# Performance work log

Measured on AMD Instinct MI355X. Metric: run time of the kernel, lower is better.

Reference implementation:

```python
import jax, jax.numpy as jnp
import numpy as np

NUM_BINS = 32
NUM_HEADS = 4
CHANNELS = 128
HEAD_DIM = CHANNELS // NUM_HEADS
SCALE = HEAD_DIM ** -0.5
BN_EPS = 1e-5


def setup_inputs() -> dict:
    key = jax.random.key(0)
    ks = jax.random.split(key, 8)
    B = 8192
    x = jax.random.normal(ks[0], (B, CHANNELS, NUM_BINS), dtype=jnp.float32)
    qkv_w = jax.random.normal(ks[1], (3 * CHANNELS, CHANNELS), dtype=jnp.float32) * (1.0 / np.sqrt(CHANNELS))
    qkv_b = jax.random.normal(ks[2], (3 * CHANNELS,), dtype=jnp.float32) * 0.01
    out_w = jax.random.normal(ks[3], (CHANNELS, CHANNELS), dtype=jnp.float32) * (1.0 / np.sqrt(CHANNELS))
    out_b = jax.random.normal(ks[4], (CHANNELS,), dtype=jnp.float32) * 0.01
    rel_pos_emb = jax.random.normal(ks[5], (2 * NUM_BINS - 1, NUM_HEADS), dtype=jnp.float32) * 0.02
    gamma = jnp.ones((CHANNELS,), dtype=jnp.float32)
    beta = jnp.zeros((CHANNELS,), dtype=jnp.float32)
    return {"x": x, "qkv_w": qkv_w, "qkv_b": qkv_b, "out_w": out_w,
            "out_b": out_b, "rel_pos_emb": rel_pos_emb, "gamma": gamma, "beta": beta}


def _rel_pos_bias(rel_pos_emb, n):
    # pos_idx[i,j] = (j - i) + num_bins - 1, clamped
    pos = jnp.arange(n)
    idx = jnp.clip(pos[None, :] - pos[:, None] + NUM_BINS - 1, 0, 2 * NUM_BINS - 2)
    bias = rel_pos_emb[idx]            # [n, n, H]
    return jnp.transpose(bias, (2, 0, 1))  # [H, n, n]


def reference(x, qkv_w, qkv_b, out_w, out_b, rel_pos_emb, gamma, beta):
    B, C, N = x.shape
    residual = x
    # 1x1 conv == per-position matmul over channels
    qkv = jnp.einsum('oc,bcn->bon', qkv_w, x) + qkv_b[None, :, None]  # [B, 3C, N]
    q, k, v = jnp.split(qkv, 3, axis=1)
    def heads(t):  # [B, C, N] -> [B, H, N, D]
        return jnp.transpose(t.reshape(B, NUM_HEADS, HEAD_DIM, N), (0, 1, 3, 2))
    q, k, v = heads(q), heads(k), heads(v)
    attn = jnp.einsum('bhnd,bhmd->bhnm', q, k) * SCALE
    attn = attn + _rel_pos_bias(rel_pos_emb, N)[None]  # [B, H, N, N]
    attn = jax.nn.softmax(attn, axis=-1)
    out = jnp.einsum('bhnm,bhmd->bhnd', attn, v)       # [B, H, N, D]
    out = jnp.transpose(out, (0, 1, 3, 2)).reshape(B, C, N)
    out = jnp.einsum('oc,bcn->bon', out_w, out) + out_b[None, :, None]
    out = out + residual
    # BatchNorm1d (training-mode batch stats, biased variance), per-channel over (B, N)
    mean = jnp.mean(out, axis=(0, 2), keepdims=True)
    var = jnp.mean((out - mean) ** 2, axis=(0, 2), keepdims=True)
    out = (out - mean) / jnp.sqrt(var + BN_EPS)
    out = out * gamma[None, :, None] + beta[None, :, None]
    return out
```

## Files before the change

### kernel.cpp

```cpp
#include <hip/hip_runtime.h>
#include <hip/hip_bf16.h>

typedef unsigned short u16;
typedef __bf16 bf16x8 __attribute__((ext_vector_type(8)));
typedef float f32x4 __attribute__((ext_vector_type(4)));

#define CH 128
#define NB 32
#define SCALE_F 0.17677669529663687f

__device__ __forceinline__ u16 f2b(float f) {
  union { float f; unsigned u; } v; v.f = f;
  unsigned r = v.u + 0x7fffu + ((v.u >> 16) & 1u);
  return (u16)(r >> 16);
}

__global__ void prep_kernel(const float* __restrict__ qw, const float* __restrict__ ow,
                            u16* __restrict__ wq, u16* __restrict__ wo,
                            float* __restrict__ stats) {
  int t = blockIdx.x * 256 + threadIdx.x;
  if (t < 49152) wq[t] = f2b(qw[t]);
  if (t < 16384) wo[t] = f2b(ow[t]);
  if (t < 8192)  stats[t] = 0.0f;
}

__global__ __launch_bounds__(256, 4) void attn_kernel(
    const float* __restrict__ x, const u16* __restrict__ wq,
    const float* __restrict__ qkv_b, const u16* __restrict__ wo,
    const float* __restrict__ out_b, const float* __restrict__ rel,
    float* __restrict__ out, float* __restrict__ stats) {

  __shared__ __attribute__((aligned(16))) u16 sQKt[32 * 256];
  __shared__ __attribute__((aligned(16))) u16 sVn[4][32 * 40];
  __shared__ __attribute__((aligned(16))) u16 sPO[4][32 * 40];

  const int tid = threadIdx.x;
  const int w = tid >> 6, lane = tid & 63;
  const int g = lane >> 4, l15 = lane & 15;
  const int b = blockIdx.x, h = w;
  const float* xb = x + (size_t)b * (CH * NB);
  const f32x4 zf = {0.f, 0.f, 0.f, 0.f};

  const float relv = rel[(lane < 63 ? lane : 62) * 4 + h];

  f32x4 acc[6][2];
  #pragma unroll
  for (int tt = 0; tt < 6; ++tt)
    #pragma unroll
    for (int ct = 0; ct < 2; ++ct) acc[tt][ct] = zf;

  #pragma unroll
  for (int kk = 0; kk < 4; ++kk) {
    bf16x8 bfr[2];
    #pragma unroll
    for (int ct = 0; ct < 2; ++ct) {
      float xv[8];
      #pragma unroll
      for (int j = 0; j < 8; ++j)
        xv[j] = xb[(kk * 32 + 8 * g + j) * NB + 16 * ct + l15];
      union { bf16x8 v; unsigned u[4]; } uu;
      #pragma unroll
      for (int m = 0; m < 4; ++m)
        uu.u[m] = (unsigned)f2b(xv[2 * m]) | ((unsigned)f2b(xv[2 * m + 1]) << 16);
      bfr[ct] = uu.v;
    }
    #pragma unroll
    for (int tt = 0; tt < 6; ++tt) {
      const int part = tt >> 1, td = tt & 1;
      const int row = part * 128 + h * 32 + 16 * td + l15;
      bf16x8 afr = *(const bf16x8*)&wq[row * 128 + kk * 32 + 8 * g];
      acc[tt][0] = __builtin_amdgcn_mfma_f32_16x16x32_bf16(afr, bfr[0], acc[tt][0], 0, 0, 0);
      acc[tt][1] = __builtin_amdgcn_mfma_f32_16x16x32_bf16(afr, bfr[1], acc[tt][1], 0, 0, 0);
    }
  }

  #pragma unroll
  for (int tt = 0; tt < 6; ++tt) {
    const int part = tt >> 1, td = tt & 1;
    #pragma unroll
    for (int r = 0; r < 4; ++r) {
      const int d = 16 * td + 4 * g + r;
      const int orow = part * 128 + h * 32 + d;
      const float bias = qkv_b[orow];
      #pragma unroll
      for (int ct = 0; ct < 2; ++ct) {
        const int n = 16 * ct + l15;
        const u16 hv = f2b(acc[tt][ct][r] + bias);
        if (part < 2) sQKt[(n * 256 + orow) ^ ((n & 7) << 3)] = hv;
        else          sVn[w][d * 40 + n] = hv;
      }
    }
  }

  bf16x8 qf[2], kf[2];
  #pragma unroll
  for (int t2 = 0; t2 < 2; ++t2) {
    const int n = 16 * t2 + l15;
    qf[t2] = *(const bf16x8*)&sQKt[(n * 256 + h * 32 + 8 * g) ^ ((n & 7) << 3)];
    kf[t2] = *(const bf16x8*)&sQKt[(n * 256 + 128 + h * 32 + 8 * g) ^ ((n & 7) << 3)];
  }
  f32x4 sacc[2][2];
  #pragma unroll
  for (int tn = 0; tn < 2; ++tn)
    #pragma unroll
    for (int tm = 0; tm < 2; ++tm)
      sacc[tn][tm] = __builtin_amdgcn_mfma_f32_16x16x32_bf16(qf[tn], kf[tm], zf, 0, 0, 0);

  u16* sPw = sPO[w];
  #pragma unroll
  for (int tn = 0; tn < 2; ++tn) {
    #pragma unroll
    for (int r = 0; r < 4; ++r) {
      const int n = 16 * tn + 4 * g + r;
      float v0 = sacc[tn][0][r] * SCALE_F + __shfl(relv, l15 - n + 31);
      float v1 = sacc[tn][1][r] * SCALE_F + __shfl(relv, 16 + l15 - n + 31);
      float mx = fmaxf(v0, v1);
      #pragma unroll
      for (int msk = 1; msk < 16; msk <<= 1) mx = fmaxf(mx, __shfl_xor(mx, msk));
      float e0 = __expf(v0 - mx), e1 = __expf(v1 - mx);
      float sm = e0 + e1;
      #pragma unroll
      for (int msk = 1; msk < 16; msk <<= 1) sm += __shfl_xor(sm, msk);
      const float ri = 1.0f / sm;
      sPw[n * 40 + l15]      = f2b(e0 * ri);
      sPw[n * 40 + 16 + l15] = f2b(e1 * ri);
    }
  }

  bf16x8 pf[2], vf[2];
  #pragma unroll
  for (int t2 = 0; t2 < 2; ++t2) {
    pf[t2] = *(const bf16x8*)&sPw[(16 * t2 + l15) * 40 + 8 * g];
    vf[t2] = *(const bf16x8*)&sVn[w][(16 * t2 + l15) * 40 + 8 * g];
  }
  f32x4 oacc[2][2];
  #pragma unroll
  for (int tn = 0; tn < 2; ++tn)
    #pragma unroll
    for (int td = 0; td < 2; ++td)
      oacc[tn][td] = __builtin_amdgcn_mfma_f32_16x16x32_bf16(pf[tn], vf[td], zf, 0, 0, 0);

  __syncthreads();

  u16* sO = &sPO[0][0];
  #pragma unroll
  for (int tn = 0; tn < 2; ++tn)
    #pragma unroll
    for (int td = 0; td < 2; ++td)
      #pragma unroll
      for (int r = 0; r < 4; ++r) {
        const int n = 16 * tn + 4 * g + r;
        const int c = h * 32 + 16 * td + l15;
        sO[(n * 128 + c) ^ ((n & 7) << 3)] = f2b(oacc[tn][td][r]);
      }

  __syncthreads();

  f32x4 pacc[2][2];
  #pragma unroll
  for (int mi = 0; mi < 2; ++mi)
    #pragma unroll
    for (int ct = 0; ct < 2; ++ct) pacc[mi][ct] = zf;

  #pragma unroll
  for (int kk = 0; kk < 4; ++kk) {
    bf16x8 bfr[2];
    #pragma unroll
    for (int ct = 0; ct < 2; ++ct) {
      const int n = 16 * ct + l15;
      bfr[ct] = *(const bf16x8*)&sO[(n * 128 + kk * 32 + 8 * g) ^ ((n & 7) << 3)];
    }
    #pragma unroll
    for (int mi = 0; mi < 2; ++mi) {
      const int row = 32 * w + 16 * mi + l15;
      bf16x8 afr = *(const bf16x8*)&wo[row * 128 + kk * 32 + 8 * g];
      pacc[mi][0] = __builtin_amdgcn_mfma_f32_16x16x32_bf16(afr, bfr[0], pacc[mi][0], 0, 0, 0);
      pacc[mi][1] = __builtin_amdgcn_mfma_f32_16x16x32_bf16(afr, bfr[1], pacc[mi][1], 0, 0, 0);
    }
  }

  float* ob = out + (size_t)b * (CH * NB);
  #pragma unroll
  for (int mi = 0; mi < 2; ++mi) {
    #pragma unroll
    for (int r = 0; r < 4; ++r) {
      const int o = 32 * w + 16 * mi + 4 * g + r;
      const float bias = out_b[o];
      float ssum = 0.f, ssq = 0.f;
      #pragma unroll
      for (int ct = 0; ct < 2; ++ct) {
        const int n = 16 * ct + l15;
        const float val = pacc[mi][ct][r] + bias + xb[o * NB + n];
        ob[o * NB + n] = val;
        ssum += val; ssq += val * val;
      }
      #pragma unroll
      for (int msk = 1; msk < 16; msk <<= 1) {
        ssum += __shfl_xor(ssum, msk);
        ssq  += __shfl_xor(ssq, msk);
      }
      if (l15 == 0) {
        atomicAdd(&stats[(b & 31) * 128 + o], ssum);
        atomicAdd(&stats[4096 + (b & 31) * 128 + o], ssq);
      }
    }
  }
}

__global__ void bnstats_kernel(const float* __restrict__ stats,
                               const float* __restrict__ gamma,
                               const float* __restrict__ beta,
                               float* __restrict__ sc, float* __restrict__ sh,
                               float invM) {
  int c = threadIdx.x;
  if (c >= 128) return;
  float s = 0.f, q = 0.f;
  #pragma unroll 8
  for (int i = 0; i < 32; ++i) {
    s += stats[i * 128 + c];
    q += stats[4096 + i * 128 + c];
  }
  float mean = s * invM;
  float var  = q * invM - mean * mean;
  float rstd = rsqrtf(var + 1e-5f);
  float a = gamma[c] * rstd;
  sc[c] = a;
  sh[c] = beta[c] - mean * a;
}

__global__ __launch_bounds__(256) void bnapply_kernel(float* __restrict__ out,
                                                      const float* __restrict__ sc,
                                                      const float* __restrict__ sh,
                                                      int n4total) {
  int i = blockIdx.x * 256 + threadIdx.x;
  int stride = gridDim.x * 256;
  for (; i < n4total; i += stride) {
    int c = (i >> 3) & 127;
    float a = sc[c], d = sh[c];
    float4 v = ((float4*)out)[i];
    v.x = v.x * a + d;
    v.y = v.y * a + d;
    v.z = v.z * a + d;
    v.w = v.w * a + d;
    ((float4*)out)[i] = v;
  }
}

extern "C" void kernel_launch(void* const* d_in, const int* in_sizes, int n_in,
                              void* d_out, int out_size, void* d_ws, size_t ws_size,
                              hipStream_t stream) {
  const float* x     = (const float*)d_in[0];
  const float* qkv_w = (const float*)d_in[1];
  const float* qkv_b = (const float*)d_in[2];
  const float* out_w = (const float*)d_in[3];
  const float* out_b = (const float*)d_in[4];
  const float* rel   = (const float*)d_in[5];
  const float* gamma = (const float*)d_in[6];
  const float* beta  = (const float*)d_in[7];
  float* out = (float*)d_out;

  const int B = in_sizes[0] / (CH * NB);

  u16* wq = (u16*)d_ws;
  u16* wo = wq + 49152;
  float* stats = (float*)(wo + 16384);
  float* sc = stats + 8192;
  float* sh = sc + 128;

  prep_kernel<<<192, 256, 0, stream>>>(qkv_w, out_w, wq, wo, stats);
  attn_kernel<<<B, 256, 0, stream>>>(x, wq, qkv_b, wo, out_b, rel, out, stats);
  bnstats_kernel<<<1, 128, 0, stream>>>(stats, gamma, beta, sc, sh, 1.0f / (float)(B * NB));
  bnapply_kernel<<<2048, 256, 0, stream>>>(out, sc, sh, out_size / 4);
}
```

Before: 430.0 us.

## Store pre-BN output as bf16 scratch, shrink LDS, transpose scores, raise occupancy

```diff
diff --git a/kernel.cpp b/kernel.cpp
--- a/kernel.cpp
+++ b/kernel.cpp
@@ -2,6 +2,7 @@
 #include <hip/hip_bf16.h>
 
 typedef unsigned short u16;
+typedef unsigned int u32;
 typedef __bf16 bf16x8 __attribute__((ext_vector_type(8)));
 typedef float f32x4 __attribute__((ext_vector_type(4)));
 
@@ -9,10 +10,12 @@
 #define NB 32
 #define SCALE_F 0.17677669529663687f
 
-__device__ __forceinline__ u16 f2b(float f) {
-  union { float f; unsigned u; } v; v.f = f;
-  unsigned r = v.u + 0x7fffu + ((v.u >> 16) & 1u);
-  return (u16)(r >> 16);
+__device__ __forceinline__ u16 b2u(__bf16 h) {
+  union { __bf16 h; u16 u; } v; v.h = h; return v.u;
+}
+__device__ __forceinline__ u16 f2b(float f) { return b2u((__bf16)f); }
+__device__ __forceinline__ u32 pk2(float lo, float hi) {
+  union { __bf16 h[2]; u32 w; } v; v.h[0] = (__bf16)lo; v.h[1] = (__bf16)hi; return v.w;
 }
 
 __global__ void prep_kernel(const float* __restrict__ qw, const float* __restrict__ ow,
@@ -24,15 +27,14 @@
   if (t < 8192)  stats[t] = 0.0f;
 }
 
-__global__ __launch_bounds__(256, 4) void attn_kernel(
+__global__ __launch_bounds__(256, 6) void attn_kernel(
     const float* __restrict__ x, const u16* __restrict__ wq,
     const float* __restrict__ qkv_b, const u16* __restrict__ wo,
     const float* __restrict__ out_b, const float* __restrict__ rel,
-    float* __restrict__ out, float* __restrict__ stats) {
-
-  __shared__ __attribute__((aligned(16))) u16 sQKt[32 * 256];
-  __shared__ __attribute__((aligned(16))) u16 sVn[4][32 * 40];
-  __shared__ __attribute__((aligned(16))) u16 sPO[4][32 * 40];
+    float* __restrict__ out, float* __restrict__ stats,
+    u16* __restrict__ preb) {
+
+  __shared__ __attribute__((aligned(16))) u16 pool[13312];
 
   const int tid = threadIdx.x;
   const int w = tid >> 6, lane = tid & 63;
@@ -41,6 +43,11 @@
   const float* xb = x + (size_t)b * (CH * NB);
   const f32x4 zf = {0.f, 0.f, 0.f, 0.f};
 
+  u16* sQKw = pool + w * 2048;
+  u16* sVw  = pool + 8192 + w * 1280;
+  u16* sPw  = sQKw;
+  u16* sO   = pool;
+
   const float relv = rel[(lane < 63 ? lane : 62) * 4 + h];
 
   f32x4 acc[6][2];
@@ -54,15 +61,9 @@
     bf16x8 bfr[2];
     #pragma unroll
     for (int ct = 0; ct < 2; ++ct) {
-      float xv[8];
       #pragma unroll
       for (int j = 0; j < 8; ++j)
-        xv[j] = xb[(kk * 32 + 8 * g + j) * NB + 16 * ct + l15];
-      union { bf16x8 v; unsigned u[4]; } uu;
-      #pragma unroll
-      for (int m = 0; m < 4; ++m)
-        uu.u[m] = (unsigned)f2b(xv[2 * m]) | ((unsigned)f2b(xv[2 * m + 1]) << 16);
-      bfr[ct] = uu.v;
+        bfr[ct][j] = (__bf16)xb[(kk * 32 + 8 * g + j) * NB + 16 * ct + l15];
     }
     #pragma unroll
     for (int tt = 0; tt < 6; ++tt) {
@@ -75,19 +76,34 @@
   }
 
   #pragma unroll
-  for (int tt = 0; tt < 6; ++tt) {
+  for (int tt = 0; tt < 4; ++tt) {
     const int part = tt >> 1, td = tt & 1;
+    #pragma unroll
+    for (int rp = 0; rp < 4; rp += 2) {
+      const int d0 = 16 * td + 4 * g + rp;
+      float b0 = qkv_b[part * 128 + h * 32 + d0];
+      float b1 = qkv_b[part * 128 + h * 32 + d0 + 1];
+      #pragma unroll
+      for (int ct = 0; ct < 2; ++ct) {
+        const int n = 16 * ct + l15;
+        float v0 = acc[tt][ct][rp]     + b0;
+        float v1 = acc[tt][ct][rp + 1] + b1;
+        if (part == 0) { v0 *= SCALE_F; v1 *= SCALE_F; }
+        const int idx = (n * 64 + part * 32 + d0) ^ ((n & 7) << 3);
+        *(u32*)&sQKw[idx] = pk2(v0, v1);
+      }
+    }
+  }
+  #pragma unroll
+  for (int td = 0; td < 2; ++td) {
     #pragma unroll
     for (int r = 0; r < 4; ++r) {
       const int d = 16 * td + 4 * g + r;
-      const int orow = part * 128 + h * 32 + d;
-      const float bias = qkv_b[orow];
+      const float bv = qkv_b[256 + h * 32 + d];
       #pragma unroll
       for (int ct = 0; ct < 2; ++ct) {
         const int n = 16 * ct + l15;
-        const u16 hv = f2b(acc[tt][ct][r] + bias);
-        if (part < 2) sQKt[(n * 256 + orow) ^ ((n & 7) << 3)] = hv;
-        else          sVn[w][d * 40 + n] = hv;
+        sVw[d * 40 + n] = f2b(acc[4 + td][ct][r] + bv);
       }
     }
   }
@@ -96,43 +112,56 @@
   #pragma unroll
   for (int t2 = 0; t2 < 2; ++t2) {
     const int n = 16 * t2 + l15;
-    qf[t2] = *(const bf16x8*)&sQKt[(n * 256 + h * 32 + 8 * g) ^ ((n & 7) << 3)];
-    kf[t2] = *(const bf16x8*)&sQKt[(n * 256 + 128 + h * 32 + 8 * g) ^ ((n & 7) << 3)];
-  }
-  f32x4 sacc[2][2];
-  #pragma unroll
-  for (int tn = 0; tn < 2; ++tn)
+    qf[t2] = *(const bf16x8*)&sQKw[(n * 64 + 8 * g)      ^ ((n & 7) << 3)];
+    kf[t2] = *(const bf16x8*)&sQKw[(n * 64 + 32 + 8 * g) ^ ((n & 7) << 3)];
+  }
+  f32x4 st[2][2];
+  #pragma unroll
+  for (int tm = 0; tm < 2; ++tm)
+    #pragma unroll
+    for (int tn = 0; tn < 2; ++tn)
+      st[tm][tn] = __builtin_amdgcn_mfma_f32_16x16x32_bf16(kf[tm], qf[tn], zf, 0, 0, 0);
+
+  #pragma unroll
+  for (int tn = 0; tn < 2; ++tn) {
+    float v[2][4];
     #pragma unroll
     for (int tm = 0; tm < 2; ++tm)
-      sacc[tn][tm] = __builtin_amdgcn_mfma_f32_16x16x32_bf16(qf[tn], kf[tm], zf, 0, 0, 0);
-
-  u16* sPw = sPO[w];
-  #pragma unroll
-  for (int tn = 0; tn < 2; ++tn) {
-    #pragma unroll
-    for (int r = 0; r < 4; ++r) {
-      const int n = 16 * tn + 4 * g + r;
-      float v0 = sacc[tn][0][r] * SCALE_F + __shfl(relv, l15 - n + 31);
-      float v1 = sacc[tn][1][r] * SCALE_F + __shfl(relv, 16 + l15 - n + 31);
-      float mx = fmaxf(v0, v1);
-      #pragma unroll
-      for (int msk = 1; msk < 16; msk <<= 1) mx = fmaxf(mx, __shfl_xor(mx, msk));
-      float e0 = __expf(v0 - mx), e1 = __expf(v1 - mx);
-      float sm = e0 + e1;
-      #pragma unroll
-      for (int msk = 1; msk < 16; msk <<= 1) sm += __shfl_xor(sm, msk);
-      const float ri = 1.0f / sm;
-      sPw[n * 40 + l15]      = f2b(e0 * ri);
-      sPw[n * 40 + 16 + l15] = f2b(e1 * ri);
-    }
+      #pragma unroll
+      for (int r = 0; r < 4; ++r) {
+        const int idx = (16 * tm + 4 * g + r) - (16 * tn + l15) + 31;
+        v[tm][r] = st[tm][tn][r] + __shfl(relv, idx);
+      }
+    float mx = fmaxf(fmaxf(fmaxf(v[0][0], v[0][1]), fmaxf(v[0][2], v[0][3])),
+                     fmaxf(fmaxf(v[1][0], v[1][1]), fmaxf(v[1][2], v[1][3])));
+    mx = fmaxf(mx, __shfl_xor(mx, 16));
+    mx = fmaxf(mx, __shfl_xor(mx, 32));
+    float e[2][4], sm = 0.f;
+    #pragma unroll
+    for (int tm = 0; tm < 2; ++tm)
+      #pragma unroll
+      for (int r = 0; r < 4; ++r) { e[tm][r] = __expf(v[tm][r] - mx); sm += e[tm][r]; }
+    sm += __shfl_xor(sm, 16);
+    sm += __shfl_xor(sm, 32);
+    const float ri = 1.0f / sm;
+    #pragma unroll
+    for (int tm = 0; tm < 2; ++tm)
+      #pragma unroll
+      for (int rp = 0; rp < 4; rp += 2) {
+        const int q = 16 * tn + l15;
+        *(u32*)&sPw[q * 40 + 16 * tm + 4 * g + rp] =
+            pk2(e[tm][rp] * ri, e[tm][rp + 1] * ri);
+      }
   }
 
   bf16x8 pf[2], vf[2];
   #pragma unroll
   for (int t2 = 0; t2 < 2; ++t2) {
     pf[t2] = *(const bf16x8*)&sPw[(16 * t2 + l15) * 40 + 8 * g];
-    vf[t2] = *(const bf16x8*)&sVn[w][(16 * t2 + l15) * 40 + 8 * g];
-  }
+    vf[t2] = *(const bf16x8*)&sVw[(16 * t2 + l15) * 40 + 8 * g];
+  }
+  __syncthreads();
+
   f32x4 oacc[2][2];
   #pragma unroll
   for (int tn = 0; tn < 2; ++tn)
@@ -140,9 +169,6 @@
     for (int td = 0; td < 2; ++td)
       oacc[tn][td] = __builtin_amdgcn_mfma_f32_16x16x32_bf16(pf[tn], vf[td], zf, 0, 0, 0);
 
-  __syncthreads();
-
-  u16* sO = &sPO[0][0];
   #pragma unroll
   for (int tn = 0; tn < 2; ++tn)
     #pragma unroll
@@ -151,7 +177,7 @@
       for (int r = 0; r < 4; ++r) {
         const int n = 16 * tn + 4 * g + r;
         const int c = h * 32 + 16 * td + l15;
-        sO[(n * 128 + c) ^ ((n & 7) << 3)] = f2b(oacc[tn][td][r]);
+        sO[n * 136 + c] = f2b(oacc[tn][td][r]);
       }
 
   __syncthreads();
@@ -166,10 +192,8 @@
   for (int kk = 0; kk < 4; ++kk) {
     bf16x8 bfr[2];
     #pragma unroll
-    for (int ct = 0; ct < 2; ++ct) {
-      const int n = 16 * ct + l15;
-      bfr[ct] = *(const bf16x8*)&sO[(n * 128 + kk * 32 + 8 * g) ^ ((n & 7) << 3)];
-    }
+    for (int ct = 0; ct < 2; ++ct)
+      bfr[ct] = *(const bf16x8*)&sO[(16 * ct + l15) * 136 + kk * 32 + 8 * g];
     #pragma unroll
     for (int mi = 0; mi < 2; ++mi) {
       const int row = 32 * w + 16 * mi + l15;
@@ -180,6 +204,7 @@
   }
 
   float* ob = out + (size_t)b * (CH * NB);
+  u16* pb = preb ? preb + (size_t)b * (CH * NB) : (u16*)0;
   #pragma unroll
   for (int mi = 0; mi < 2; ++mi) {
     #pragma unroll
@@ -191,7 +216,8 @@
       for (int ct = 0; ct < 2; ++ct) {
         const int n = 16 * ct + l15;
         const float val = pacc[mi][ct][r] + bias + xb[o * NB + n];
-        ob[o * NB + n] = val;
+        if (pb) pb[o * NB + n] = f2b(val);
+        else    ob[o * NB + n] = val;
         ssum += val; ssq += val * val;
       }
       #pragma unroll
@@ -246,6 +272,25 @@
   }
 }
 
+__global__ __launch_bounds__(256) void bnapply_bf16_kernel(
+    const u16* __restrict__ preb, float* __restrict__ out,
+    const float* __restrict__ sc, const float* __restrict__ sh, int n4total) {
+  int i = blockIdx.x * 256 + threadIdx.x;
+  int stride = gridDim.x * 256;
+  for (; i < n4total; i += stride) {
+    int c = (i >> 3) & 127;
+    float a = sc[c], d = sh[c];
+    uint2 u = ((const uint2*)preb)[i];
+    float4 v;
+    union { u32 w; float f; } t;
+    t.w = (u.x & 0xffffu) << 16; v.x = t.f * a + d;
+    t.w = (u.x & 0xffff0000u);   v.y = t.f * a + d;
+    t.w = (u.y & 0xffffu) << 16; v.z = t.f * a + d;
+    t.w = (u.y & 0xffff0000u);   v.w = t.f * a + d;
+    ((float4*)out)[i] = v;
+  }
+}
+
 extern "C" void kernel_launch(void* const* d_in, const int* in_sizes, int n_in,
                               void* d_out, int out_size, void* d_ws, size_t ws_size,
                               hipStream_t stream) {
@@ -266,9 +311,18 @@
   float* stats = (float*)(wo + 16384);
   float* sc = stats + 8192;
   float* sh = sc + 128;
+  u16* preb = (u16*)(sh + 128);
+
+  const size_t need = (size_t)(49152 + 16384) * 2 + (size_t)8448 * 4
+                    + (size_t)B * CH * NB * 2;
+  const bool useB16 = ws_size >= need;
 
   prep_kernel<<<192, 256, 0, stream>>>(qkv_w, out_w, wq, wo, stats);
-  attn_kernel<<<B, 256, 0, stream>>>(x, wq, qkv_b, wo, out_b, rel, out, stats);
+  attn_kernel<<<B, 256, 0, stream>>>(x, wq, qkv_b, wo, out_b, rel, out, stats,
+                                     useB16 ? preb : (u16*)0);
   bnstats_kernel<<<1, 128, 0, stream>>>(stats, gamma, beta, sc, sh, 1.0f / (float)(B * NB));
-  bnapply_kernel<<<2048, 256, 0, stream>>>(out, sc, sh, out_size / 4);
-}
+  if (useB16)
+    bnapply_bf16_kernel<<<2048, 256, 0, stream>>>(preb, out, sc, sh, out_size / 4);
+  else
+    bnapply_kernel<<<2048, 256, 0, stream>>>(out, sc, sh, out_size / 4);
+}
```

New measurement: 538.0 us. +25.1%, slower.
